# Performance work log

Measured on AMD Instinct MI355X. Metric: run time of the kernel, lower is better.

## Reference

```python
import jax, jax.numpy as jnp
import numpy as np

# Config (DiffWave-style)
C = 64        # channels
K = 3         # kernel_size
L = 30        # num_layers
CYCLES = 3    # num_cycles
DRATE = 2     # dilation_rate
ITER = 50     # diffusion steps
ESIZE = 128   # embedding_size
EPROJ = 512   # embedding_proj
EFACT = 4.0   # embedding_factor
B, T = 4, 16384
LAYERS_PER_CYCLE = L // CYCLES
DILATIONS = [DRATE ** (i % LAYERS_PER_CYCLE) for i in range(L)]
INV_SQRT2 = 1.0 / np.sqrt(2.0).astype(np.float32)


def _embed_table():
    # [ITER, ESIZE] sinusoidal noise-schedule embedding (deterministic buffer)
    logit = jnp.linspace(0.0, 1.0, ESIZE // 2)
    exp = jnp.power(10.0, logit * EFACT)
    t = jnp.arange(1, ITER + 1, dtype=jnp.float32)
    comp = exp[None, :] * t[:, None]
    return jnp.concatenate([jnp.sin(comp), jnp.cos(comp)], axis=-1)


def _dconv(x, w, d):
    # x: [B,T,Cin], w: [K,Cin,Cout], SAME padding, dilation d -> [B,T,Cout]
    return jax.lax.conv_general_dilated(
        x, w, window_strides=(1,), padding='SAME', rhs_dilation=(d,),
        dimension_numbers=('NWC', 'WIO', 'NWC'))


def setup_inputs() -> dict:
    key = jax.random.key(0)
    ks = jax.random.split(key, 20)
    g = lambda k, shape, fan_in: (jax.random.normal(k, shape) / np.sqrt(fan_in)).astype(jnp.float32)
    return {
        'signal': jax.random.normal(ks[0], (B, T), dtype=jnp.float32),
        'timestep': jax.random.randint(ks[1], (B,), 1, ITER + 1, dtype=jnp.int32),
        'in_w': g(ks[2], (1, C), 1),
        'in_b': jnp.zeros((C,), jnp.float32),
        'pe0_w': g(ks[3], (ESIZE, EPROJ), ESIZE),
        'pe0_b': jnp.zeros((EPROJ,), jnp.float32),
        'pe1_w': g(ks[4], (EPROJ, EPROJ), EPROJ),
        'pe1_b': jnp.zeros((EPROJ,), jnp.float32),
        'blk_emb_w': g(ks[5], (L, EPROJ, C), EPROJ),
        'blk_emb_b': jnp.zeros((L, C), jnp.float32),
        'blk_conv_w': g(ks[6], (L, K, C, 2 * C), K * C),
        'blk_conv_b': jnp.zeros((L, 2 * C), jnp.float32),
        'blk_res_w': g(ks[7], (L - 1, C, C), C),
        'blk_res_b': jnp.zeros((L - 1, C), jnp.float32),
        'blk_skip_w': g(ks[8], (L, C, C), C),
        'blk_skip_b': jnp.zeros((L, C), jnp.float32),
        'out0_w': g(ks[9], (C, C), C),
        'out0_b': jnp.zeros((C,), jnp.float32),
        'out1_w': g(ks[10], (C, 1), C),
        'out1_b': jnp.zeros((1,), jnp.float32),
    }


def reference(signal, timestep, in_w, in_b, pe0_w, pe0_b, pe1_w, pe1_b,
              blk_emb_w, blk_emb_b, blk_conv_w, blk_conv_b,
              blk_res_w, blk_res_b, blk_skip_w, blk_skip_b,
              out0_w, out0_b, out1_w, out1_b):
    # input 1x1 conv + relu: [B,T] -> [B,T,C]
    x = jax.nn.relu(signal[..., None] * in_w[0][None, None, :] + in_b)
    # noise-schedule embedding [B,ESIZE] -> swish MLP -> [B,EPROJ]
    embed = _embed_table()[timestep - 1]
    embed = jax.nn.swish(embed @ pe0_w + pe0_b)
    embed = jax.nn.swish(embed @ pe1_w + pe1_b)
    skip_sum = jnp.zeros_like(x)
    for i in range(L):
        e = embed @ blk_emb_w[i] + blk_emb_b[i]           # [B,C]
        h = x + e[:, None, :]                              # [B,T,C]
        y = _dconv(h, blk_conv_w[i], DILATIONS[i]) + blk_conv_b[i]  # [B,T,2C]
        z = jnp.tanh(y[..., :C]) * jax.nn.sigmoid(y[..., C:])       # gated
        if i < L - 1:
            x = (z @ blk_res_w[i] + blk_res_b[i] + x) * INV_SQRT2
        skip_sum = skip_sum + (z @ blk_skip_w[i] + blk_skip_b[i])
    ctx = skip_sum / np.sqrt(L).astype(np.float32)
    ctx = jax.nn.relu(ctx @ out0_w + out0_b)
    out = ctx @ out1_w + out1_b                            # [B,T,1]
    return jnp.squeeze(out, axis=-1)
```

## Files before the change

kernel.cpp:

```cpp
#include <hip/hip_runtime.h>
#include <math.h>

#define TT 16384
#define BB 4
#define CC 64
#define LL 30

typedef _Float16 f16;
typedef _Float16 f16x4 __attribute__((ext_vector_type(4)));
typedef _Float16 f16x8 __attribute__((ext_vector_type(8)));
typedef float f32x4 __attribute__((ext_vector_type(4)));
typedef unsigned int u32;

#define MFMA(a, b, c) __builtin_amdgcn_mfma_f32_16x16x32_f16(a, b, c, 0, 0, 0)

__device__ __forceinline__ float fsig(float x) { return 1.0f / (1.0f + __expf(-x)); }
__device__ __forceinline__ float ftanhf(float x) { return 1.0f - 2.0f / (__expf(2.0f * x) + 1.0f); }

__device__ __forceinline__ void gl_lds16(const void* g, void* l) {
    __builtin_amdgcn_global_load_lds((const __attribute__((address_space(1))) u32*)g,
                                     (__attribute__((address_space(3))) u32*)l, 16, 0, 0);
}

__global__ void pack_weights(const float* __restrict__ conv_w, const float* __restrict__ res_w,
                             const float* __restrict__ skip_w, const float* __restrict__ out0_w,
                             f16* __restrict__ wcv, f16* __restrict__ wrs, f16* __restrict__ wsk,
                             f16* __restrict__ wo0) {
    const int total_c = LL * 6 * 8 * 64 * 8;
    const int total_r = (LL - 1) * 2 * 4 * 64 * 8;
    const int total_s = LL * 2 * 4 * 64 * 8;
    const int total_o = 2 * 4 * 64 * 8;
    const int total = total_c + total_r + total_s + total_o;
    for (int i = blockIdx.x * blockDim.x + threadIdx.x; i < total; i += gridDim.x * blockDim.x) {
        if (i < total_c) {
            int e = i & 7, lane = (i >> 3) & 63, mf = (i >> 9) & 7, rest = i >> 12;
            int ks = rest % 6, l = rest / 6;
            int cin = (ks & 1) * 32 + (lane >> 4) * 8 + e;
            int tap = ks >> 1;
            int cout = mf * 16 + (lane & 15);
            wcv[i] = (f16)conv_w[(((size_t)l * 3 + tap) * 64 + cin) * 128 + cout];
        } else if (i < total_c + total_r) {
            int j = i - total_c;
            int e = j & 7, lane = (j >> 3) & 63, mf = (j >> 9) & 3, kk = (j >> 11) & 1, l = j >> 12;
            int cin = kk * 32 + (lane >> 4) * 8 + e;
            int cout = mf * 16 + (lane & 15);
            wrs[j] = (f16)res_w[((size_t)l * 64 + cin) * 64 + cout];
        } else if (i < total_c + total_r + total_s) {
            int j = i - total_c - total_r;
            int e = j & 7, lane = (j >> 3) & 63, mf = (j >> 9) & 3, kk = (j >> 11) & 1, l = j >> 12;
            int cin = kk * 32 + (lane >> 4) * 8 + e;
            int cout = mf * 16 + (lane & 15);
            wsk[j] = (f16)skip_w[((size_t)l * 64 + cin) * 64 + cout];
        } else {
            int j = i - total_c - total_r - total_s;
            int e = j & 7, lane = (j >> 3) & 63, mf = (j >> 9) & 3, kk = (j >> 11) & 1;
            int cin = kk * 32 + (lane >> 4) * 8 + e;
            int c = mf * 16 + (lane & 15);
            wo0[j] = (f16)out0_w[cin * 64 + c];
        }
    }
}

__global__ void init_x_kernel(const float* __restrict__ signal, const float* __restrict__ in_w,
                              const float* __restrict__ in_b, f16* __restrict__ x0) {
    int i = blockIdx.x * 256 + threadIdx.x;
    int bt = i >> 3, g = i & 7;
    float s = signal[bt];
    f32x4 w0 = *(const f32x4*)&in_w[g * 8];
    f32x4 w1 = *(const f32x4*)&in_w[g * 8 + 4];
    f32x4 b0 = *(const f32x4*)&in_b[g * 8];
    f32x4 b1 = *(const f32x4*)&in_b[g * 8 + 4];
    f16x8 o;
#pragma unroll
    for (int j = 0; j < 4; ++j) {
        o[j] = (f16)fmaxf(s * w0[j] + b0[j], 0.f);
        o[4 + j] = (f16)fmaxf(s * w1[j] + b1[j], 0.f);
    }
    *(f16x8*)&x0[(size_t)bt * CC + g * 8] = o;
}

__global__ void embed_stage1(const int* __restrict__ timestep, const float* __restrict__ pe0_w,
                             const float* __restrict__ pe0_b, float* __restrict__ h1) {
    __shared__ float emb[BB * 128];
    __shared__ float red[256];
    const int tid = threadIdx.x;
    for (int i = tid; i < BB * 128; i += 256) {
        int b = i >> 7, j = i & 127, jj = j & 63;
        float logit = (jj == 63) ? 1.0f : (float)jj * (1.0f / 63.0f);
        double e10 = pow(10.0, (double)(4.0f * logit));
        float comp = (float)e10 * (float)timestep[b];
        emb[i] = (j < 64) ? (float)sin((double)comp) : (float)cos((double)comp);
    }
    __syncthreads();
    const int c16 = tid & 15, b = (tid >> 4) & 3, part = tid >> 6;
    const int col = blockIdx.x * 16 + c16;
    float s = 0.f;
#pragma unroll
    for (int j = part * 32; j < part * 32 + 32; ++j)
        s += emb[b * 128 + j] * pe0_w[j * 512 + col];
    red[tid] = s;
    __syncthreads();
    if (part == 0) {
        float x = red[tid] + red[tid + 64] + red[tid + 128] + red[tid + 192] + pe0_b[col];
        h1[b * 512 + col] = x * fsig(x);
    }
}

__global__ void embed_stage2(const float* __restrict__ h1, const float* __restrict__ pe1_w,
                             const float* __restrict__ pe1_b, float* __restrict__ embed2) {
    __shared__ float hs[BB * 512];
    __shared__ float red[256];
    const int tid = threadIdx.x;
    for (int i = tid; i < BB * 512; i += 256) hs[i] = h1[i];
    __syncthreads();
    const int c8 = tid & 7, b = (tid >> 3) & 3, part = tid >> 5;
    const int col = blockIdx.x * 8 + c8;
    float s = 0.f;
#pragma unroll
    for (int j = part * 64; j < part * 64 + 64; ++j)
        s += hs[b * 512 + j] * pe1_w[j * 512 + col];
    red[tid] = s;
    __syncthreads();
    if (part == 0) {
        float x = pe1_b[col];
#pragma unroll
        for (int ph = 0; ph < 8; ++ph) x += red[ph * 32 + (tid & 31)];
        embed2[b * 512 + col] = x * fsig(x);
    }
}

__global__ void e_kernel(const float* __restrict__ embed2, const float* __restrict__ blk_emb_w,
                         const float* __restrict__ blk_emb_b, float* __restrict__ e_out) {
    const int l = blockIdx.x, b = blockIdx.y;
    const int tid = threadIdx.x;
    __shared__ float em[512];
    __shared__ float red[256];
    for (int i = tid; i < 512; i += 256) em[i] = embed2[b * 512 + i];
    __syncthreads();
    const int c = tid & 63, part = tid >> 6;
    float s0 = 0.f, s1 = 0.f;
    for (int j = part * 128; j < part * 128 + 128; j += 2) {
        s0 += em[j] * blk_emb_w[((size_t)l * 512 + j) * 64 + c];
        s1 += em[j + 1] * blk_emb_w[((size_t)l * 512 + j + 1) * 64 + c];
    }
    red[tid] = s0 + s1;
    __syncthreads();
    if (tid < 64)
        e_out[(l * BB + b) * 64 + tid] =
            red[tid] + red[tid + 64] + red[tid + 128] + red[tid + 192] + blk_emb_b[l * 64 + tid];
}

__global__ void evec2_kernel(const float* __restrict__ e_in, const float* __restrict__ conv_w,
                             const float* __restrict__ conv_b, float* __restrict__ evec) {
    const int l = blockIdx.x, tap = blockIdx.y, b = blockIdx.z;
    const int n = threadIdx.x;
    __shared__ float es[64];
    if (n < 64) es[n] = e_in[(l * BB + b) * 64 + n];
    __syncthreads();
    const float* cw = conv_w + ((size_t)(l * 3 + tap) * 64) * 128;
    float a0 = 0.f, a1 = 0.f, a2 = 0.f, a3 = 0.f;
#pragma unroll
    for (int k = 0; k < 64; k += 4) {
        a0 += es[k] * cw[k * 128 + n];
        a1 += es[k + 1] * cw[(k + 1) * 128 + n];
        a2 += es[k + 2] * cw[(k + 2) * 128 + n];
        a3 += es[k + 3] * cw[(k + 3) * 128 + n];
    }
    float s = a0 + a1 + a2 + a3 + ((tap == 1) ? conv_b[l * 128 + n] : 0.f);
    evec[((size_t)(l * 4 + b) * 3 + tap) * 128 + n] = s;
}

__global__ void sbsum_kernel(const float* __restrict__ skip_b, float* __restrict__ sbsum) {
    int c = threadIdx.x;
    float s = 0.f;
    for (int l = 0; l < LL; ++l) s += skip_b[l * 64 + c];
    sbsum[c] = s;
}

__launch_bounds__(256, 5)
__global__ void layer_kernel(const f16* __restrict__ xin, f16* __restrict__ xout,
                             f16* __restrict__ zg,
                             const f16* __restrict__ wcv, const f16* __restrict__ wrs,
                             const float* __restrict__ evec_l, const float* __restrict__ res_b,
                             const f16* __restrict__ zpage, int d) {
    extern __shared__ f16 lds[];
    const int tid = threadIdx.x, lane = tid & 63, w = tid >> 6;
    const int lrow = lane & 15, lk = lane >> 4;
    const int lin = blockIdx.x;
    const int lin2 = (lin & 7) * 128 + (lin >> 3);
    const int b = lin2 >> 8, t0 = (lin2 & 255) * 64;
    const int stride = (d < 64) ? d : 64;
    const int R8 = (64 + 2 * stride + 7) & ~7;
    f16* xs = lds;
    f16* zs = lds + R8 * 64;
    const f16* xb = xin + (size_t)b * TT * CC;
    f16* zb = zg + (size_t)b * TT * CC;

    const int NCH = R8 >> 3;
    for (int chunk = w; chunk < NCH; chunk += 4) {
        int gid = chunk * 64 + lane;
        int r = gid >> 3, g = gid & 7;
        int t = t0 - d + r + ((d > 64) ? ((r >> 6) * (d - 64)) : 0);
        const f16* src = ((unsigned)t < TT) ? (xb + (size_t)t * CC + ((g ^ (r & 7)) << 3)) : zpage;
        gl_lds16(src, (void*)((char*)xs + chunk * 1024));
    }
    __syncthreads();

    f32x4 acc[2][4] = {};
#pragma unroll
    for (int ks = 0; ks < 6; ++ks) {
        const int tap = ks >> 1, kk = ks & 1;
        f16x8 aw0 = *(const f16x8*)&wcv[((ks * 8 + w) * 64 + lane) * 8];
        f16x8 aw1 = *(const f16x8*)&wcv[((ks * 8 + w + 4) * 64 + lane) * 8];
#pragma unroll
        for (int nfi = 0; nfi < 4; ++nfi) {
            int r = nfi * 16 + lrow + tap * stride;
            int g = kk * 4 + lk;
            f16x8 bx = *(const f16x8*)&xs[r * 64 + ((g ^ (r & 7)) << 3)];
            acc[0][nfi] = MFMA(aw0, bx, acc[0][nfi]);
            acc[1][nfi] = MFMA(aw1, bx, acc[1][nfi]);
        }
    }

    const float* evb = evec_l + b * 384;
    const int ca = w * 16 + lk * 4;
    const int gz = ca >> 3;
    f32x4 e0a = *(const f32x4*)&evb[ca], e1a = *(const f32x4*)&evb[128 + ca],
          e2a = *(const f32x4*)&evb[256 + ca];
    f32x4 e0b = *(const f32x4*)&evb[64 + ca], e1b = *(const f32x4*)&evb[192 + ca],
          e2b = *(const f32x4*)&evb[320 + ca];
#pragma unroll
    for (int nfi = 0; nfi < 4; ++nfi) {
        int trow = nfi * 16 + lrow;
        int t = t0 + trow;
        float m0 = (t >= d) ? 1.f : 0.f;
        float m2 = (t + d < TT) ? 1.f : 0.f;
        f16x4 zo;
#pragma unroll
        for (int r = 0; r < 4; ++r) {
            float ya = acc[0][nfi][r] + e1a[r] + m0 * e0a[r] + m2 * e2a[r];
            float yb = acc[1][nfi][r] + e1b[r] + m0 * e0b[r] + m2 * e2b[r];
            zo[r] = (f16)(ftanhf(ya) * fsig(yb));
        }
        *(f16x4*)&zs[trow * 64 + ((gz ^ (trow & 7)) << 3) + (ca & 7)] = zo;
        *(f16x4*)&zb[(size_t)(t0 + trow) * CC + ca] = zo;
    }

    if (wrs != nullptr) {
        __syncthreads();
        f32x4 accR[4] = {};
#pragma unroll
        for (int kk = 0; kk < 2; ++kk) {
            f16x8 ar_ = *(const f16x8*)&wrs[((kk * 4 + w) * 64 + lane) * 8];
#pragma unroll
            for (int nfi = 0; nfi < 4; ++nfi) {
                int trow = nfi * 16 + lrow;
                int g = kk * 4 + lk;
                f16x8 bz = *(const f16x8*)&zs[trow * 64 + ((g ^ (trow & 7)) << 3)];
                accR[nfi] = MFMA(ar_, bz, accR[nfi]);
            }
        }
        f16* xob = xout + (size_t)b * TT * CC;
        f32x4 rb4 = *(const f32x4*)&res_b[ca];
#pragma unroll
        for (int nfi = 0; nfi < 4; ++nfi) {
            int trow = nfi * 16 + lrow;
            int rr = stride + trow;
            f16x4 xv = *(const f16x4*)&xs[rr * 64 + ((gz ^ (rr & 7)) << 3) + (ca & 7)];
            f16x4 xo;
#pragma unroll
            for (int r = 0; r < 4; ++r)
                xo[r] = (f16)((accR[nfi][r] + rb4[r] + (float)xv[r]) * 0.70710678118654752f);
            *(f16x4*)&xob[(size_t)(t0 + trow) * CC + ca] = xo;
        }
    }
}

__launch_bounds__(256)
__global__ void skip_head(const f16* __restrict__ zbuf, const f16* __restrict__ z29,
                          const f16* __restrict__ wsk, const f16* __restrict__ wo0,
                          const float* __restrict__ sbsum, const float* __restrict__ out0_b,
                          const float* __restrict__ out1_w, const float* __restrict__ out1_b,
                          float* __restrict__ out) {
    __shared__ f16 zb[2][64 * 64];
    const int tid = threadIdx.x, lane = tid & 63, w = tid >> 6;
    const int lrow = lane & 15, lk = lane >> 4;
    const int lin = blockIdx.x;
    const int lin2 = (lin & 7) * 128 + (lin >> 3);
    const int b = lin2 >> 8, tile = lin2 & 255;
    const int t0 = tile * 64;

#define STAGE_Z(L, BUF)                                                                       \
    {                                                                                         \
        const f16* zl =                                                                       \
            (((L) < LL - 1) ? (zbuf + (size_t)(L)*BB * TT * CC) : z29) + (size_t)b * TT * CC; \
        _Pragma("unroll") for (int j = 0; j < 2; ++j) {                                       \
            int chunk = j * 4 + w;                                                            \
            int gid = chunk * 64 + lane;                                                      \
            int r = gid >> 3, g = gid & 7;                                                    \
            gl_lds16(zl + (size_t)(t0 + r) * CC + ((g ^ (r & 7)) << 3),                       \
                     (void*)((char*)zb[BUF] + chunk * 1024));                                 \
        }                                                                                     \
    }

    f32x4 accS[4] = {};
    STAGE_Z(0, 0);
    for (int l = 0; l < LL; ++l) {
        __syncthreads();
        if (l + 1 < LL) STAGE_Z(l + 1, (l + 1) & 1);
        const f16* wl = wsk + (size_t)l * 4096;
        const f16* zcur = zb[l & 1];
#pragma unroll
        for (int kk = 0; kk < 2; ++kk) {
            f16x8 as_ = *(const f16x8*)&wl[((kk * 4 + w) * 64 + lane) * 8];
#pragma unroll
            for (int nt = 0; nt < 4; ++nt) {
                int trow = nt * 16 + lrow;
                int g = kk * 4 + lk;
                f16x8 bz = *(const f16x8*)&zcur[trow * 64 + ((g ^ (trow & 7)) << 3)];
                accS[nt] = MFMA(as_, bz, accS[nt]);
            }
        }
    }

    __syncthreads();
    const float invL = 0.18257418583505537f;
    const int cb = w * 16 + lk * 4;
    const int gz = cb >> 3;
    f32x4 sb4 = *(const f32x4*)&sbsum[cb];
#pragma unroll
    for (int nt = 0; nt < 4; ++nt) {
        int row = nt * 16 + lrow;
        f16x4 sn;
#pragma unroll
        for (int r = 0; r < 4; ++r) sn[r] = (f16)((accS[nt][r] + sb4[r]) * invL);
        *(f16x4*)&zb[0][row * 64 + ((gz ^ (row & 7)) << 3) + (cb & 7)] = sn;
    }
    __syncthreads();

    const int trow = w * 16 + lrow;
    f32x4 accO[4] = {};
#pragma unroll
    for (int kk = 0; kk < 2; ++kk) {
        int g = kk * 4 + lk;
        f16x8 bz = *(const f16x8*)&zb[0][trow * 64 + ((g ^ (trow & 7)) << 3)];
#pragma unroll
        for (int mf = 0; mf < 4; ++mf) {
            f16x8 aw = *(const f16x8*)&wo0[((kk * 4 + mf) * 64 + lane) * 8];
            accO[mf] = MFMA(aw, bz, accO[mf]);
        }
    }
    float pv = 0.f;
    const float b1 = out1_b[0];
#pragma unroll
    for (int mf = 0; mf < 4; ++mf) {
        int c = mf * 16 + lk * 4;
        f32x4 b0 = *(const f32x4*)&out0_b[c];
        f32x4 w1 = *(const f32x4*)&out1_w[c];
#pragma unroll
        for (int r = 0; r < 4; ++r) pv += fmaxf(accO[mf][r] + b0[r], 0.f) * w1[r];
    }
    pv += __shfl_xor(pv, 16);
    pv += __shfl_xor(pv, 32);
    if (lane < 16) out[(size_t)b * TT + t0 + w * 16 + lane] = pv + b1;
#undef STAGE_Z
}

extern "C" void kernel_launch(void* const* d_in, const int* in_sizes, int n_in,
                              void* d_out, int out_size, void* d_ws, size_t ws_size,
                              hipStream_t stream) {
    const float* signal = (const float*)d_in[0];
    const int* timestep = (const int*)d_in[1];
    const float* in_w = (const float*)d_in[2];
    const float* in_b = (const float*)d_in[3];
    const float* pe0_w = (const float*)d_in[4];
    const float* pe0_b = (const float*)d_in[5];
    const float* pe1_w = (const float*)d_in[6];
    const float* pe1_b = (const float*)d_in[7];
    const float* blk_emb_w = (const float*)d_in[8];
    const float* blk_emb_b = (const float*)d_in[9];
    const float* blk_conv_w = (const float*)d_in[10];
    const float* blk_conv_b = (const float*)d_in[11];
    const float* blk_res_w = (const float*)d_in[12];
    const float* blk_res_b = (const float*)d_in[13];
    const float* blk_skip_w = (const float*)d_in[14];
    const float* blk_skip_b = (const float*)d_in[15];
    const float* out0_w = (const float*)d_in[16];
    const float* out0_b = (const float*)d_in[17];
    const float* out1_w = (const float*)d_in[18];
    const float* out1_b = (const float*)d_in[19];

    char* p = (char*)d_ws;
    const size_t xhsz = (size_t)BB * TT * CC * sizeof(f16);
    const size_t BTC = (size_t)BB * TT * CC;
    f16* xa = (f16*)p; p += xhsz;
    f16* xb2 = (f16*)p; p += xhsz;
    f16* wcv = (f16*)p; p += (size_t)737280 * 2;
    f16* wrs = (f16*)p; p += (size_t)118784 * 2;
    f16* wsk = (f16*)p; p += (size_t)122880 * 2;
    f16* wo0 = (f16*)p; p += (size_t)4096 * 2;
    float* h1 = (float*)p; p += 4 * 512 * sizeof(float);
    float* embed2 = (float*)p; p += 4 * 512 * sizeof(float);
    float* e_buf = (float*)p; p += (size_t)LL * BB * 64 * sizeof(float);
    float* evec = (float*)p; p += (size_t)LL * 4 * 3 * 128 * sizeof(float);
    float* sbsum = (float*)p; p += 64 * sizeof(float);
    f16* zpage = (f16*)p; p += 256;
    p = (char*)(((size_t)p + 255) & ~(size_t)255);
    f16* zbuf = (f16*)p; p += (size_t)(LL - 1) * xhsz;

    hipMemsetAsync(zpage, 0, 256, stream);
    pack_weights<<<1024, 256, 0, stream>>>(blk_conv_w, blk_res_w, blk_skip_w, out0_w,
                                           wcv, wrs, wsk, wo0);
    init_x_kernel<<<2048, 256, 0, stream>>>(signal, in_w, in_b, xa);
    embed_stage1<<<32, 256, 0, stream>>>(timestep, pe0_w, pe0_b, h1);
    embed_stage2<<<64, 256, 0, stream>>>(h1, pe1_w, pe1_b, embed2);
    e_kernel<<<dim3(LL, BB), 256, 0, stream>>>(embed2, blk_emb_w, blk_emb_b, e_buf);
    evec2_kernel<<<dim3(LL, 3, BB), 128, 0, stream>>>(e_buf, blk_conv_w, blk_conv_b, evec);
    sbsum_kernel<<<1, 64, 0, stream>>>(blk_skip_b, sbsum);

    f16* cur = xa;
    f16* nxt = xb2;
    f16* z29 = xa;
    for (int i = 0; i < LL; ++i) {
        int d = 1 << (i % 10);
        bool last = (i == LL - 1);
        f16* zg = last ? nxt : (zbuf + (size_t)i * BTC);
        if (last) z29 = nxt;
        int stride = (d < 64) ? d : 64;
        int R8 = (64 + 2 * stride + 7) & ~7;
        size_t smem = (size_t)(R8 * 64 + 64 * 64) * sizeof(f16);
        layer_kernel<<<BB * (TT / 64), 256, smem, stream>>>(
            cur, nxt, zg, wcv + (size_t)i * 24576,
            last ? nullptr : (wrs + (size_t)i * 4096), evec + (size_t)i * 1536,
            last ? nullptr : (blk_res_b + i * 64), zpage, d);
        if (!last) { f16* t = cur; cur = nxt; nxt = t; }
    }

    skip_head<<<(BB * TT) / 64, 256, 0, stream>>>(zbuf, z29, wsk, wo0, sbsum, out0_b, out1_w,
                                                  out1_b, (float*)d_out);
}
```

Before: 480.3 us.

## Fuse consecutive small-dilation layer pairs into one kernel with halo recompute

Adds a templated pair_kernel that computes two consecutive residual layers (dilations 1,2 and 4,8 of each cycle) in one launch. It loads a wider halo tile of x, computes the first layer's gated output and residual over the extended range in shared memory, then runs the second layer from shared memory. This removes one global write and read of the intermediate x and one launch per pair, cutting 6 of 30 layer launches. In exchange it recomputes the halo rows and uses more shared memory and registers per block.

```diff
diff --git a/kernel.cpp b/kernel.cpp
--- a/kernel.cpp
+++ b/kernel.cpp
@@ -276,6 +276,187 @@
     }
 }
 
+template <int D1, int D2>
+__launch_bounds__(256, 4)
+__global__ void pair_kernel(const f16* __restrict__ xin, f16* __restrict__ xout,
+                            f16* __restrict__ zg1, f16* __restrict__ zg2,
+                            const f16* __restrict__ wcv1, const f16* __restrict__ wcv2,
+                            const f16* __restrict__ wrs1, const f16* __restrict__ wrs2,
+                            const float* __restrict__ evec1, const float* __restrict__ evec2,
+                            const float* __restrict__ resb1, const float* __restrict__ resb2,
+                            const f16* __restrict__ zpage) {
+    constexpr int H = D1 + D2;
+    constexpr int RX = 64 + 2 * H;
+    constexpr int R8X = (RX + 7) & ~7;
+    constexpr int NT = (RX + 15) / 16;
+    constexpr int ZR = NT * 16;
+    __shared__ f16 xs[R8X * 64];
+    __shared__ f16 zs[ZR * 64];
+    __shared__ f16 xn[ZR * 64];
+    f16* z2 = xs;
+
+    const int tid = threadIdx.x, lane = tid & 63, w = tid >> 6;
+    const int lrow = lane & 15, lk = lane >> 4;
+    const int lin = blockIdx.x;
+    const int lin2 = (lin & 7) * 128 + (lin >> 3);
+    const int b = lin2 >> 8, t0 = (lin2 & 255) * 64;
+    const f16* xb = xin + (size_t)b * TT * CC;
+    f16* zb1 = zg1 + (size_t)b * TT * CC;
+    f16* zb2 = zg2 + (size_t)b * TT * CC;
+    f16* xob = xout + (size_t)b * TT * CC;
+    const int ca = w * 16 + lk * 4, gz = ca >> 3;
+
+    const int NCH = R8X >> 3;
+    for (int chunk = w; chunk < NCH; chunk += 4) {
+        int gid = chunk * 64 + lane;
+        int r = gid >> 3, g = gid & 7;
+        int t = t0 - H + r;
+        const f16* src = ((unsigned)t < TT) ? (xb + (size_t)t * CC + ((g ^ (r & 7)) << 3)) : zpage;
+        gl_lds16(src, (void*)((char*)xs + chunk * 1024));
+    }
+    __syncthreads();
+
+    {
+        f32x4 acc[2][NT] = {};
+#pragma unroll
+        for (int ks = 0; ks < 6; ++ks) {
+            const int tap = ks >> 1, kk = ks & 1;
+            f16x8 aw0 = *(const f16x8*)&wcv1[((ks * 8 + w) * 64 + lane) * 8];
+            f16x8 aw1 = *(const f16x8*)&wcv1[((ks * 8 + w + 4) * 64 + lane) * 8];
+#pragma unroll
+            for (int nfi = 0; nfi < NT; ++nfi) {
+                int rx = nfi * 16 + lrow + (tap - 1) * D1;
+                rx = (rx < 0) ? 0 : ((rx > R8X - 1) ? (R8X - 1) : rx);
+                int g = kk * 4 + lk;
+                f16x8 bx = *(const f16x8*)&xs[rx * 64 + ((g ^ (rx & 7)) << 3)];
+                acc[0][nfi] = MFMA(aw0, bx, acc[0][nfi]);
+                acc[1][nfi] = MFMA(aw1, bx, acc[1][nfi]);
+            }
+        }
+        const float* evb = evec1 + b * 384;
+        f32x4 e0a = *(const f32x4*)&evb[ca], e1a = *(const f32x4*)&evb[128 + ca],
+              e2a = *(const f32x4*)&evb[256 + ca];
+        f32x4 e0b = *(const f32x4*)&evb[64 + ca], e1b = *(const f32x4*)&evb[192 + ca],
+              e2b = *(const f32x4*)&evb[320 + ca];
+#pragma unroll
+        for (int nfi = 0; nfi < NT; ++nfi) {
+            int rt = nfi * 16 + lrow;
+            int tz = t0 - H + rt;
+            bool valid = ((unsigned)tz < TT);
+            float m0 = (tz >= D1) ? 1.f : 0.f;
+            float m2 = (tz + D1 < TT) ? 1.f : 0.f;
+            f16x4 zo;
+#pragma unroll
+            for (int r = 0; r < 4; ++r) {
+                float ya = acc[0][nfi][r] + e1a[r] + m0 * e0a[r] + m2 * e2a[r];
+                float yb = acc[1][nfi][r] + e1b[r] + m0 * e0b[r] + m2 * e2b[r];
+                zo[r] = valid ? (f16)(ftanhf(ya) * fsig(yb)) : (f16)0;
+            }
+            *(f16x4*)&zs[rt * 64 + ((gz ^ (rt & 7)) << 3) + (ca & 7)] = zo;
+            if (rt >= H && rt < H + 64) *(f16x4*)&zb1[(size_t)tz * CC + ca] = zo;
+        }
+    }
+    __syncthreads();
+
+    {
+        f32x4 accR[NT] = {};
+#pragma unroll
+        for (int kk = 0; kk < 2; ++kk) {
+            f16x8 ar_ = *(const f16x8*)&wrs1[((kk * 4 + w) * 64 + lane) * 8];
+#pragma unroll
+            for (int nfi = 0; nfi < NT; ++nfi) {
+                int rt = nfi * 16 + lrow;
+                int g = kk * 4 + lk;
+                f16x8 bz = *(const f16x8*)&zs[rt * 64 + ((g ^ (rt & 7)) << 3)];
+                accR[nfi] = MFMA(ar_, bz, accR[nfi]);
+            }
+        }
+        f32x4 rb4 = *(const f32x4*)&resb1[ca];
+#pragma unroll
+        for (int nfi = 0; nfi < NT; ++nfi) {
+            int rt = nfi * 16 + lrow;
+            int tz = t0 - H + rt;
+            bool valid = ((unsigned)tz < TT);
+            int rxc = (rt > R8X - 1) ? (R8X - 1) : rt;
+            f16x4 xv = *(const f16x4*)&xs[rxc * 64 + ((gz ^ (rxc & 7)) << 3) + (ca & 7)];
+            f16x4 xo;
+#pragma unroll
+            for (int r = 0; r < 4; ++r)
+                xo[r] = valid ? (f16)((accR[nfi][r] + rb4[r] + (float)xv[r]) * 0.70710678118654752f)
+                              : (f16)0;
+            *(f16x4*)&xn[rt * 64 + ((gz ^ (rt & 7)) << 3) + (ca & 7)] = xo;
+        }
+    }
+    __syncthreads();
+
+    {
+        f32x4 acc[2][4] = {};
+#pragma unroll
+        for (int ks = 0; ks < 6; ++ks) {
+            const int tap = ks >> 1, kk = ks & 1;
+            f16x8 aw0 = *(const f16x8*)&wcv2[((ks * 8 + w) * 64 + lane) * 8];
+            f16x8 aw1 = *(const f16x8*)&wcv2[((ks * 8 + w + 4) * 64 + lane) * 8];
+#pragma unroll
+            for (int nfi = 0; nfi < 4; ++nfi) {
+                int rxn = nfi * 16 + lrow + H + (tap - 1) * D2;
+                int g = kk * 4 + lk;
+                f16x8 bx = *(const f16x8*)&xn[rxn * 64 + ((g ^ (rxn & 7)) << 3)];
+                acc[0][nfi] = MFMA(aw0, bx, acc[0][nfi]);
+                acc[1][nfi] = MFMA(aw1, bx, acc[1][nfi]);
+            }
+        }
+        const float* evb = evec2 + b * 384;
+        f32x4 e0a = *(const f32x4*)&evb[ca], e1a = *(const f32x4*)&evb[128 + ca],
+              e2a = *(const f32x4*)&evb[256 + ca];
+        f32x4 e0b = *(const f32x4*)&evb[64 + ca], e1b = *(const f32x4*)&evb[192 + ca],
+              e2b = *(const f32x4*)&evb[320 + ca];
+#pragma unroll
+        for (int nfi = 0; nfi < 4; ++nfi) {
+            int trow = nfi * 16 + lrow;
+            int t = t0 + trow;
+            float m0 = (t >= D2) ? 1.f : 0.f;
+            float m2 = (t + D2 < TT) ? 1.f : 0.f;
+            f16x4 zo;
+#pragma unroll
+            for (int r = 0; r < 4; ++r) {
+                float ya = acc[0][nfi][r] + e1a[r] + m0 * e0a[r] + m2 * e2a[r];
+                float yb = acc[1][nfi][r] + e1b[r] + m0 * e0b[r] + m2 * e2b[r];
+                zo[r] = (f16)(ftanhf(ya) * fsig(yb));
+            }
+            *(f16x4*)&z2[trow * 64 + ((gz ^ (trow & 7)) << 3) + (ca & 7)] = zo;
+            *(f16x4*)&zb2[(size_t)t * CC + ca] = zo;
+        }
+    }
+    __syncthreads();
+
+    {
+        f32x4 accR[4] = {};
+#pragma unroll
+        for (int kk = 0; kk < 2; ++kk) {
+            f16x8 ar_ = *(const f16x8*)&wrs2[((kk * 4 + w) * 64 + lane) * 8];
+#pragma unroll
+            for (int nfi = 0; nfi < 4; ++nfi) {
+                int trow = nfi * 16 + lrow;
+                int g = kk * 4 + lk;
+                f16x8 bz = *(const f16x8*)&z2[trow * 64 + ((g ^ (trow & 7)) << 3)];
+                accR[nfi] = MFMA(ar_, bz, accR[nfi]);
+            }
+        }
+        f32x4 rb4 = *(const f32x4*)&resb2[ca];
+#pragma unroll
+        for (int nfi = 0; nfi < 4; ++nfi) {
+            int trow = nfi * 16 + lrow;
+            int rr = trow + H;
+            f16x4 xv = *(const f16x4*)&xn[rr * 64 + ((gz ^ (rr & 7)) << 3) + (ca & 7)];
+            f16x4 xo;
+#pragma unroll
+            for (int r = 0; r < 4; ++r)
+                xo[r] = (f16)((accR[nfi][r] + rb4[r] + (float)xv[r]) * 0.70710678118654752f);
+            *(f16x4*)&xob[(size_t)(t0 + trow) * CC + ca] = xo;
+        }
+    }
+}
+
 __launch_bounds__(256)
 __global__ void skip_head(const f16* __restrict__ zbuf, const f16* __restrict__ z29,
                           const f16* __restrict__ wsk, const f16* __restrict__ wo0,
@@ -421,19 +602,36 @@
     f16* cur = xa;
     f16* nxt = xb2;
     f16* z29 = xa;
-    for (int i = 0; i < LL; ++i) {
-        int d = 1 << (i % 10);
-        bool last = (i == LL - 1);
-        f16* zg = last ? nxt : (zbuf + (size_t)i * BTC);
-        if (last) z29 = nxt;
-        int stride = (d < 64) ? d : 64;
-        int R8 = (64 + 2 * stride + 7) & ~7;
-        size_t smem = (size_t)(R8 * 64 + 64 * 64) * sizeof(f16);
-        layer_kernel<<<BB * (TT / 64), 256, smem, stream>>>(
-            cur, nxt, zg, wcv + (size_t)i * 24576,
-            last ? nullptr : (wrs + (size_t)i * 4096), evec + (size_t)i * 1536,
-            last ? nullptr : (blk_res_b + i * 64), zpage, d);
-        if (!last) { f16* t = cur; cur = nxt; nxt = t; }
+    for (int c = 0; c < 3; ++c) {
+        const int l0 = c * 10;
+        pair_kernel<1, 2><<<1024, 256, 0, stream>>>(
+            cur, nxt, zbuf + (size_t)l0 * BTC, zbuf + (size_t)(l0 + 1) * BTC,
+            wcv + (size_t)l0 * 24576, wcv + (size_t)(l0 + 1) * 24576,
+            wrs + (size_t)l0 * 4096, wrs + (size_t)(l0 + 1) * 4096,
+            evec + (size_t)l0 * 1536, evec + (size_t)(l0 + 1) * 1536,
+            blk_res_b + l0 * 64, blk_res_b + (l0 + 1) * 64, zpage);
+        { f16* t = cur; cur = nxt; nxt = t; }
+        pair_kernel<4, 8><<<1024, 256, 0, stream>>>(
+            cur, nxt, zbuf + (size_t)(l0 + 2) * BTC, zbuf + (size_t)(l0 + 3) * BTC,
+            wcv + (size_t)(l0 + 2) * 24576, wcv + (size_t)(l0 + 3) * 24576,
+            wrs + (size_t)(l0 + 2) * 4096, wrs + (size_t)(l0 + 3) * 4096,
+            evec + (size_t)(l0 + 2) * 1536, evec + (size_t)(l0 + 3) * 1536,
+            blk_res_b + (l0 + 2) * 64, blk_res_b + (l0 + 3) * 64, zpage);
+        { f16* t = cur; cur = nxt; nxt = t; }
+        for (int i = l0 + 4; i < l0 + 10; ++i) {
+            int d = 1 << (i % 10);
+            bool last = (i == LL - 1);
+            f16* zg = last ? nxt : (zbuf + (size_t)i * BTC);
+            if (last) z29 = nxt;
+            int stride = (d < 64) ? d : 64;
+            int R8 = (64 + 2 * stride + 7) & ~7;
+            size_t smem = (size_t)(R8 * 64 + 64 * 64) * sizeof(f16);
+            layer_kernel<<<BB * (TT / 64), 256, smem, stream>>>(
+                cur, nxt, zg, wcv + (size_t)i * 24576,
+                last ? nullptr : (wrs + (size_t)i * 4096), evec + (size_t)i * 1536,
+                last ? nullptr : (blk_res_b + i * 64), zpage, d);
+            if (!last) { f16* t = cur; cur = nxt; nxt = t; }
+        }
     }
 
     skip_head<<<(BB * TT) / 64, 256, 0, stream>>>(zbuf, z29, wsk, wo0, sbsum, out0_b, out1_w,
```

New measurement: 475.2 us, median of 3. About the same (-1.1%).
